# Performance work log

Hardware: AMD Instinct MI355X
Metric: run time of the kernel (lower is better)

Reference implementation:

```python
import jax, jax.numpy as jnp
import numpy as np

B, S, H, NH, HD = 2, 2048, 1024, 16, 64
RD = 16            # rotary_dim = head_dim * 0.25
W = 16             # mini_context_length (sliding window)
SCALE = HD ** -0.5
ROPE_BASE = 10000.0


def setup_inputs() -> dict:
    key = jax.random.key(0)
    ks = jax.random.split(key, 10)
    p = lambda k, shape: (jax.random.normal(k, shape, dtype=jnp.float32) * 0.02)
    return {
        "hidden_states": jax.random.normal(ks[0], (B, S, H), dtype=jnp.float32),
        "Wqkv": p(ks[1], (3 * H, H)), "bqkv": p(ks[2], (3 * H,)),
        "Wqa": p(ks[3], (H, H)),      "bqa": p(ks[4], (H,)),
        "Wka": p(ks[5], (H, H)),      "bka": p(ks[6], (H,)),
        "Wd": p(ks[7], (H, H)),       "bd": p(ks[8], (H,)),
    }


def _rotate_half(x):
    x1, x2 = jnp.split(x, 2, axis=-1)
    return jnp.concatenate([-x2, x1], axis=-1)


def _apply_rope(q, k, seq_len):
    # GPT-NeoX style rotary on the first RD dims. q,k: [B,NH,S,RD]
    inv_freq = 1.0 / (ROPE_BASE ** (jnp.arange(0, RD, 2, dtype=jnp.float32) / RD))
    t = jnp.arange(seq_len, dtype=jnp.float32)
    freqs = jnp.outer(t, inv_freq)                     # [S, RD//2]
    emb = jnp.concatenate([freqs, freqs], axis=-1)     # [S, RD]
    cos = jnp.cos(emb)[None, None]                      # [1,1,S,RD]
    sin = jnp.sin(emb)[None, None]
    return q * cos + _rotate_half(q) * sin, k * cos + _rotate_half(k) * sin


def reference(hidden_states, Wqkv, bqkv, Wqa, bqa, Wka, bka, Wd, bd):
    b, s, _ = hidden_states.shape
    qkv = hidden_states @ Wqkv.T + bqkv                       # [B,S,3H]
    qkv = qkv.reshape(b, s, 3, NH, HD).transpose(2, 0, 3, 1, 4)
    q, k, v = qkv[0], qkv[1], qkv[2]                          # [B,NH,S,HD]

    q_rot, k_rot = _apply_rope(q[..., :RD], k[..., :RD], s)
    q = jnp.concatenate([q_rot, q[..., RD:]], axis=-1)
    k = jnp.concatenate([k_rot, k[..., RD:]], axis=-1)

    # ----- Stage 1: sliding-window local attention (vectorized) -----
    pos = jnp.arange(s)
    idx = pos[:, None] - (W - 1) + jnp.arange(W)[None, :]     # [S,W]
    valid = idx >= 0
    idxc = jnp.clip(idx, 0, s - 1)
    k_win = k[:, :, idxc, :]                                   # [B,NH,S,W,HD]
    v_win = v[:, :, idxc, :]
    scores = jnp.einsum('bhsd,bhswd->bhsw', q, k_win) * SCALE
    scores = jnp.where(valid[None, None], scores, -jnp.inf)
    probs = jax.nn.softmax(scores, axis=-1)
    A = jnp.einsum('bhsw,bhswd->bhsd', probs, v_win)           # [B,NH,S,HD]

    A_hidden = A.transpose(0, 2, 1, 3).reshape(b, s, H)        # [B,S,H]

    # ----- Stage 2: causal global attention over A -----
    qa = (A_hidden @ Wqa.T + bqa).reshape(b, s, NH, HD).transpose(0, 2, 1, 3)
    ka = (A_hidden @ Wka.T + bka).reshape(b, s, NH, HD).transpose(0, 2, 1, 3)
    g = jnp.einsum('bhqd,bhkd->bhqk', qa, ka) * SCALE          # [B,NH,S,S]
    causal = pos[:, None] >= pos[None, :]
    g = jnp.where(causal[None, None], g, -jnp.inf)
    pg = jax.nn.softmax(g, axis=-1)
    out = jnp.einsum('bhqk,bhkd->bhqd', pg, A)                 # [B,NH,S,HD]
    out = out.transpose(0, 2, 1, 3).reshape(b, s, H)
    return out @ Wd.T + bd
```

## Files before the change

kernel.cpp:

```cpp
#include <hip/hip_runtime.h>
#include <hip/hip_bf16.h>
#include <cstdint>
#include <cstddef>

typedef __bf16 bf16;
typedef __bf16 bf16x4 __attribute__((ext_vector_type(4)));
typedef __bf16 bf16x8 __attribute__((ext_vector_type(8)));
typedef float  f32x4  __attribute__((ext_vector_type(4)));

#define DEVINL __device__ __forceinline__

constexpr int   Bc  = 2, Sc = 2048, Hc = 1024, NHc = 16, HDc = 64;
constexpr int   Tc  = Bc * Sc;
constexpr float L2E = 1.44269504088896340736f;
constexpr float NEG_BIG = -1.0e30f;

typedef __attribute__((address_space(1))) void AS1void;
typedef __attribute__((address_space(3))) void AS3void;

DEVINL void load_lds16(const bf16* g, bf16* l) {
  __builtin_amdgcn_global_load_lds((AS1void*)g, (AS3void*)l, 16, 0, 0);
}


__global__ __launch_bounds__(256)
void convert_all(const float* __restrict__ hs, const float* __restrict__ Wqkv,
                 const float* __restrict__ Wqa, const float* __restrict__ Wka,
                 const float* __restrict__ Wd, const float* __restrict__ bqa,
                 const float* __restrict__ bka,
                 bf16* __restrict__ hsb, bf16* __restrict__ wqkvb,
                 bf16* __restrict__ wqakab, bf16* __restrict__ wdb,
                 float* __restrict__ bqaka) {
  const int blk = blockIdx.x;
  if (blk >= 5120) {
    const int i = threadIdx.x * 8;
    const float* src = (i < 1024) ? (bqa + i) : (bka + i - 1024);
    *(f32x4*)(bqaka + i)     = *(const f32x4*)src;
    *(f32x4*)(bqaka + i + 4) = *(const f32x4*)(src + 4);
    return;
  }
  const float* src; bf16* dst; int base;
  if      (blk < 2048) { src = hs;   dst = hsb;                    base = blk; }
  else if (blk < 3584) { src = Wqkv; dst = wqkvb;                  base = blk - 2048; }
  else if (blk < 4096) { src = Wqa;  dst = wqakab;                 base = blk - 3584; }
  else if (blk < 4608) { src = Wka;  dst = wqakab + 1024 * 1024;   base = blk - 4096; }
  else                 { src = Wd;   dst = wdb;                    base = blk - 4608; }
  const int i = (base * 256 + threadIdx.x) * 8;
  f32x4 a = *(const f32x4*)(src + i);
  f32x4 b = *(const f32x4*)(src + i + 4);
  bf16x8 v;
#pragma unroll
  for (int j = 0; j < 4; j++) { v[j] = (bf16)a[j]; v[4 + j] = (bf16)b[j]; }
  *(bf16x8*)(dst + i) = v;
}

template <typename CT>
__global__ __launch_bounds__(256, 3)
void gemm128(const bf16* __restrict__ A, const bf16* __restrict__ Bw,
             const float* __restrict__ bias, CT* __restrict__ C,
             int M, int N, int K) {
  __shared__ __attribute__((aligned(16))) bf16 As[128 * 64];
  __shared__ __attribute__((aligned(16))) bf16 Bs[128 * 64];

  const int tid = threadIdx.x, wv = tid >> 6, lane = tid & 63;
  const int m0 = blockIdx.y * 128, n0 = blockIdx.x * 128;
  const int col = lane & 15, quad = lane >> 4;
  const int wrow = (wv >> 1) * 64, wcol = (wv & 1) * 64;

  f32x4 acc[4][4];
#pragma unroll
  for (int i = 0; i < 4; i++)
#pragma unroll
    for (int j = 0; j < 4; j++) acc[i][j] = f32x4{0.f, 0.f, 0.f, 0.f};

  const int srow = tid >> 3;
  const int scol = (((tid & 7) ^ (srow & 7)) << 3);
  const bf16* Ag = A  + (size_t)(m0 + srow) * K + scol;
  const bf16* Bg = Bw + (size_t)(n0 + srow) * K + scol;
  const int cs = col & 7;

  for (int k0 = 0; k0 < K; k0 += 64) {
#pragma unroll
    for (int c = 0; c < 4; c++) {
      load_lds16(Ag + (size_t)(c * 32) * K + k0, As + c * 2048 + tid * 8);
      load_lds16(Bg + (size_t)(c * 32) * K + k0, Bs + c * 2048 + tid * 8);
    }
    __syncthreads();
#pragma unroll
    for (int kk = 0; kk < 64; kk += 32) {
      const int so = ((((kk >> 3) + quad) ^ cs) << 3);
      bf16x8 af[4], bfr[4];
#pragma unroll
      for (int i = 0; i < 4; i++)
        af[i] = *(const bf16x8*)(As + (wrow + i * 16 + col) * 64 + so);
#pragma unroll
      for (int j = 0; j < 4; j++)
        bfr[j] = *(const bf16x8*)(Bs + (wcol + j * 16 + col) * 64 + so);
#pragma unroll
      for (int i = 0; i < 4; i++)
#pragma unroll
        for (int j = 0; j < 4; j++)
          acc[i][j] = __builtin_amdgcn_mfma_f32_16x16x32_bf16(af[i], bfr[j], acc[i][j], 0, 0, 0);
    }
    __syncthreads();
  }

#pragma unroll
  for (int j = 0; j < 4; j++) {
    const int c = n0 + wcol + j * 16 + col;
    const float bv = bias[c];
#pragma unroll
    for (int i = 0; i < 4; i++)
#pragma unroll
      for (int r = 0; r < 4; r++) {
        const int rr = m0 + wrow + i * 16 + quad * 4 + r;
        C[(size_t)rr * N + c] = (CT)(acc[i][j][r] + bv);
      }
  }
}

template <typename CT>
__global__ __launch_bounds__(256, 4)
void gemm6464(const bf16* __restrict__ A, const bf16* __restrict__ Bw,
              const float* __restrict__ bias, CT* __restrict__ C,
              int M, int N, int K) {
  __shared__ __attribute__((aligned(16))) bf16 As[64 * 64];
  __shared__ __attribute__((aligned(16))) bf16 Bs[64 * 64];

  const int tid = threadIdx.x, wv = tid >> 6, lane = tid & 63;
  const int m0 = blockIdx.y * 64, n0 = blockIdx.x * 64;
  const int col = lane & 15, quad = lane >> 4;

  f32x4 acc[4];
#pragma unroll
  for (int j = 0; j < 4; j++) acc[j] = f32x4{0.f, 0.f, 0.f, 0.f};

  const int srow = tid >> 3;
  const int scol = (((tid & 7) ^ (srow & 7)) << 3);
  const bf16* Ag = A  + (size_t)(m0 + srow) * K + scol;
  const bf16* Bg = Bw + (size_t)(n0 + srow) * K + scol;
  const int cs = col & 7;

  for (int k0 = 0; k0 < K; k0 += 64) {
#pragma unroll
    for (int c = 0; c < 2; c++) {
      load_lds16(Ag + (size_t)(c * 32) * K + k0, As + c * 2048 + tid * 8);
      load_lds16(Bg + (size_t)(c * 32) * K + k0, Bs + c * 2048 + tid * 8);
    }
    __syncthreads();
#pragma unroll
    for (int kk = 0; kk < 64; kk += 32) {
      const int so = ((((kk >> 3) + quad) ^ cs) << 3);
      bf16x8 af = *(const bf16x8*)(As + (wv * 16 + col) * 64 + so);
#pragma unroll
      for (int j = 0; j < 4; j++) {
        bf16x8 bfr = *(const bf16x8*)(Bs + (j * 16 + col) * 64 + so);
        acc[j] = __builtin_amdgcn_mfma_f32_16x16x32_bf16(af, bfr, acc[j], 0, 0, 0);
      }
    }
    __syncthreads();
  }

#pragma unroll
  for (int j = 0; j < 4; j++) {
    const int c = n0 + j * 16 + col;
    const float bv = bias[c];
#pragma unroll
    for (int r = 0; r < 4; r++) {
      const int rr = m0 + wv * 16 + quad * 4 + r;
      C[(size_t)rr * N + c] = (CT)(acc[j][r] + bv);
    }
  }
}

__global__ __launch_bounds__(256)
void window_attn(const bf16* __restrict__ qkv, bf16* __restrict__ Ah,
                 bf16* __restrict__ VTg) {
  __shared__ __attribute__((aligned(16))) bf16 Kw[31 * 72];
  __shared__ __attribute__((aligned(16))) bf16 Vw[31 * 72];
  const int g  = blockIdx.x;
  const int st = g & 127;
  const int h  = (g >> 7) & 15;
  const int b  = g >> 11;
  const int s0 = st * 16;
  const int tid = threadIdx.x;

  if ((tid < 124) || (tid >= 128 && tid < 252)) {
    const bool isK = tid < 124;
    const int lt  = isK ? tid : tid - 128;
    const int r   = lt >> 2, off = (lt & 3) << 4;
    int sidx = s0 - 15 + r; if (sidx < 0) sidx = 0;
    const bf16* src = qkv + (size_t)(b * Sc + sidx) * 3072 + (isK ? 1024 : 2048) + h * 64 + off;
    bf16x8 v0 = *(const bf16x8*)src;
    bf16x8 v1 = *(const bf16x8*)(src + 8);
    if (isK && off == 0) {
#pragma unroll
      for (int j = 0; j < 8; j++) {
        const float invf = exp2f(-(float)j * 1.66096404744368128f);
        float sn, csn;
        sincosf((float)sidx * invf, &sn, &csn);
        const float x1 = (float)v0[j], x2 = (float)v1[j];
        v0[j] = (bf16)(x1 * csn - x2 * sn);
        v1[j] = (bf16)(x2 * csn + x1 * sn);
      }
    }
    bf16* dst = (isK ? Kw : Vw) + r * 72 + off;
    *(bf16x8*)dst       = v0;
    *(bf16x8*)(dst + 8) = v1;
  }
  __syncthreads();

  const int wv = tid >> 6, lane = tid & 63;
  const int subq = lane >> 4, lane16 = lane & 15;
  const int s = s0 + wv * 4 + subq;
  const int t = b * Sc + s;
  const int d0 = lane16 * 4;

  float qd[4];
  {
    bf16x4 qv = *(const bf16x4*)(qkv + (size_t)t * 3072 + h * 64 + d0);
#pragma unroll
    for (int j = 0; j < 4; j++) qd[j] = (float)qv[j];
  }
  float pd[4];
#pragma unroll
  for (int j = 0; j < 4; j++) pd[j] = __shfl_xor(qd[j], 2, 64);
  if (lane16 < 4) {
#pragma unroll
    for (int j = 0; j < 4; j++) {
      const int jabs = d0 + j;
      const float invf = exp2f(-(float)(jabs & 7) * 1.66096404744368128f);
      float sn, csn;
      sincosf((float)s * invf, &sn, &csn);
      qd[j] = (jabs < 8) ? (qd[j] * csn - pd[j] * sn) : (qd[j] * csn + pd[j] * sn);
    }
  }

  float sc[16];
#pragma unroll
  for (int w = 0; w < 16; w++) {
    const int idxp = s - 15 + w;
    const int row = idxp - s0 + 15;
    bf16x4 kv = *(const bf16x4*)(Kw + row * 72 + d0);
    float p = qd[0] * (float)kv[0] + qd[1] * (float)kv[1] +
              qd[2] * (float)kv[2] + qd[3] * (float)kv[3];
#pragma unroll
    for (int m = 1; m < 16; m <<= 1) p += __shfl_xor(p, m, 64);
    sc[w] = (idxp < 0) ? NEG_BIG : p * 0.125f;
  }
  float mx = sc[0];
#pragma unroll
  for (int w = 1; w < 16; w++) mx = fmaxf(mx, sc[w]);
  float sum = 0.f;
#pragma unroll
  for (int w = 0; w < 16; w++) { sc[w] = exp2f((sc[w] - mx) * L2E); sum += sc[w]; }
  const float inv = 1.0f / fmaxf(sum, 1e-30f);

  float acc[4] = {0.f, 0.f, 0.f, 0.f};
#pragma unroll
  for (int w = 0; w < 16; w++) {
    const int idxp = s - 15 + w;
    const int row = idxp - s0 + 15;
    bf16x4 vv = *(const bf16x4*)(Vw + row * 72 + d0);
#pragma unroll
    for (int j = 0; j < 4; j++) acc[j] += sc[w] * (float)vv[j];
  }
  bf16x4 ov;
#pragma unroll
  for (int j = 0; j < 4; j++) ov[j] = (bf16)(acc[j] * inv);
  *(bf16x4*)(Ah + (size_t)t * 1024 + h * 64 + d0) = ov;
  bf16* vt = VTg + (((size_t)(b * 16 + h)) * 64 + d0) * 2048 + s;
#pragma unroll
  for (int j = 0; j < 4; j++) vt[(size_t)j * 2048] = ov[j];
}

__global__ __launch_bounds__(256, 4)
void flash_attn(const bf16* __restrict__ Q, const bf16* __restrict__ Kt,
                const bf16* __restrict__ VTg, bf16* __restrict__ O) {
  constexpr int QS = 2048;
  constexpr float SHIFT = 16.0f;
  __shared__ __attribute__((aligned(16))) bf16 K_lds[128 * 64];
  __shared__ __attribute__((aligned(16))) bf16 VT_lds[64 * 128];

  const int tid = threadIdx.x, wv = tid >> 6, lane = tid & 63;
  const int bh = blockIdx.x;
  const int y  = blockIdx.y;
  const int gq = y & 7, kq = y >> 3;
  const int qt = (kq == 0) ? gq : (kq == 1) ? (15 - gq)
               : (kq == 2) ? (16 + gq) : (31 - gq);
  const int b = bh >> 4, h = bh & 15;
  const int col = lane & 15, quad = lane >> 4;
  const size_t bS = (size_t)b * Sc;
  const int hd = h * 64;

  const int krow = tid >> 3;
  const int kcol = (((tid & 7) ^ (krow & 7)) << 3);
  const int vrow = tid >> 4;
  const int vcol = (((tid & 15) ^ vrow) << 3);
  const int cs8 = col & 7;

  const int qbase = qt * 64 + wv * 16;
  const int nkt = (qt + 2) >> 1;

  const bf16* qptr = Q + (bS + qbase + col) * QS + hd + quad * 8;
  bf16x8 qf[2];
  qf[0] = *(const bf16x8*)qptr;
  qf[1] = *(const bf16x8*)(qptr + 32);
#pragma unroll
  for (int hh = 0; hh < 2; hh++)
#pragma unroll
    for (int j = 0; j < 8; j++) qf[hh][j] = (bf16)((float)qf[hh][j] * 0.125f);

  f32x4 oacc[4];
#pragma unroll
  for (int i = 0; i < 4; i++) oacc[i] = f32x4{0.f, 0.f, 0.f, 0.f};
  float lsum = 0.f;

  for (int kt0 = 0; kt0 < nkt; kt0++) {
    const int k0 = kt0 * 128;
#pragma unroll
    for (int c = 0; c < 4; c++) {
      load_lds16(Kt + (bS + k0 + c * 32 + krow) * QS + hd + kcol,
                 K_lds + c * 2048 + tid * 8);
      load_lds16(VTg + ((size_t)bh * 64 + c * 16 + vrow) * 2048 + k0 + vcol,
                 VT_lds + c * 2048 + tid * 8);
    }
    __syncthreads();

    f32x4 sacc[8];
#pragma unroll
    for (int sub = 0; sub < 8; sub++) {
      f32x4 a = f32x4{0.f, 0.f, 0.f, 0.f};
#pragma unroll
      for (int hh = 0; hh < 2; hh++) {
        const int so = (((hh * 4 + quad) ^ cs8) << 3);
        bf16x8 kf = *(const bf16x8*)(K_lds + (sub * 16 + col) * 64 + so);
        a = __builtin_amdgcn_mfma_f32_16x16x32_bf16(kf, qf[hh], a, 0, 0, 0);
      }
      sacc[sub] = a;
    }
    if (kt0 == nkt - 1) {
      const int qq = qbase + col;
#pragma unroll
      for (int sub = 0; sub < 8; sub++)
#pragma unroll
        for (int r = 0; r < 4; r++) {
          const int key = k0 + sub * 16 + quad * 4 + r;
          if (key > qq) sacc[sub][r] = NEG_BIG;
        }
    }
#pragma unroll
    for (int sub = 0; sub < 8; sub++)
#pragma unroll
      for (int r = 0; r < 4; r++) {
        sacc[sub][r] = exp2f(sacc[sub][r] * L2E - SHIFT);
        lsum += sacc[sub][r];
      }

#pragma unroll
    for (int t = 0; t < 4; t++) {
      uint32_t a0, a1, b0, b1;
      asm("v_cvt_pk_bf16_f32 %0, %1, %2"
          : "=v"(a0) : "v"(sacc[2 * t][0]), "v"(sacc[2 * t][1]));
      asm("v_cvt_pk_bf16_f32 %0, %1, %2"
          : "=v"(a1) : "v"(sacc[2 * t][2]), "v"(sacc[2 * t][3]));
      asm("v_cvt_pk_bf16_f32 %0, %1, %2"
          : "=v"(b0) : "v"(sacc[2 * t + 1][0]), "v"(sacc[2 * t + 1][1]));
      asm("v_cvt_pk_bf16_f32 %0, %1, %2"
          : "=v"(b1) : "v"(sacc[2 * t + 1][2]), "v"(sacc[2 * t + 1][3]));
      asm("v_permlane32_swap_b32 %0, %1" : "+v"(a0), "+v"(b0));
      asm("v_permlane16_swap_b32 %0, %1" : "+v"(a0), "+v"(b0));
      asm("v_permlane32_swap_b32 %0, %1" : "+v"(a1), "+v"(b1));
      asm("v_permlane16_swap_b32 %0, %1" : "+v"(a1), "+v"(b1));
      union { uint32_t u[4]; bf16x8 v; } pk;
      pk.u[0] = a0; pk.u[1] = a1; pk.u[2] = b0; pk.u[3] = b1;
      const int vso = (((4 * t + quad) ^ col) << 3);
#pragma unroll
      for (int nb = 0; nb < 4; nb++) {
        bf16x8 vf = *(const bf16x8*)(VT_lds + (nb * 16 + col) * 128 + vso);
        oacc[nb] = __builtin_amdgcn_mfma_f32_16x16x32_bf16(pk.v, vf, oacc[nb], 0, 0, 0);
      }
    }
    __syncthreads();
  }

  float tot = lsum;
  tot += __shfl_xor(tot, 16, 64);
  tot += __shfl_xor(tot, 32, 64);
  float lrow[4];
#pragma unroll
  for (int r = 0; r < 4; r++)
    lrow[r] = 1.0f / fmaxf(__shfl(tot, quad * 4 + r, 16), 1e-37f);

#pragma unroll
  for (int nb = 0; nb < 4; nb++)
#pragma unroll
    for (int r = 0; r < 4; r++) {
      const int qq = qbase + quad * 4 + r;
      O[(bS + qq) * 1024 + hd + nb * 16 + col] = (bf16)(oacc[nb][r] * lrow[r]);
    }
}

extern "C" void kernel_launch(void* const* d_in, const int* in_sizes, int n_in,
                              void* d_out, int out_size, void* d_ws, size_t ws_size,
                              hipStream_t stream) {
  (void)in_sizes; (void)n_in; (void)out_size; (void)ws_size;
  const float* hs   = (const float*)d_in[0];
  const float* Wqkv = (const float*)d_in[1];
  const float* bqkv = (const float*)d_in[2];
  const float* Wqa  = (const float*)d_in[3];
  const float* bqa  = (const float*)d_in[4];
  const float* Wka  = (const float*)d_in[5];
  const float* bka  = (const float*)d_in[6];
  const float* Wd   = (const float*)d_in[7];
  const float* bd   = (const float*)d_in[8];
  float* out = (float*)d_out;

  const size_t TH = (size_t)Tc * Hc;
  bf16* dob   = (bf16*)d_out;
  bf16* hsb   = dob;
  bf16* wqkvb = dob + TH;
  bf16* Ah    = dob;
  bf16* VTg   = dob + TH;
  bf16* ws     = (bf16*)d_ws;
  bf16* qkv    = ws;
  bf16* qaka   = ws;
  bf16* oh     = ws + 2 * TH;
  bf16* wqakab = ws + 3 * TH;
  bf16* wdb    = wqakab + 2 * 1024 * 1024;
  float* bqaka = (float*)(wdb + 1024 * 1024);

  convert_all<<<dim3(5121), 256, 0, stream>>>(hs, Wqkv, Wqa, Wka, Wd, bqa, bka,
                                              hsb, wqkvb, wqakab, wdb, bqaka);

  gemm128<bf16><<<dim3(24, 32), 256, 0, stream>>>(hsb, wqkvb, bqkv, qkv, Tc, 3 * Hc, Hc);
  window_attn<<<dim3(Tc * NHc / 16), 256, 0, stream>>>(qkv, Ah, VTg);
  gemm128<bf16><<<dim3(16, 32), 256, 0, stream>>>(Ah, wqakab, bqaka, qaka, Tc, 2 * Hc, Hc);
  flash_attn<<<dim3(Bc * NHc, 32), 256, 0, stream>>>(qaka, qaka + Hc, VTg, oh);
  gemm6464<float><<<dim3(16, 64), 256, 0, stream>>>(oh, wdb, bd, out, Tc, Hc, Hc);
}
```

Before: 225.0 us.

## Pair complementary query tiles per block and double-buffer K/V tiles in LDS

Each flash-attention block now processes two query tiles, y and 31-y, so every block runs a constant 17 key-tile iterations. This balances the causal triangle across blocks and halves the grid. The K and V^T LDS buffers are doubled so the next tile's async global-to-LDS load is issued before computing on the current one, overlapping memory with MFMA work. In exchange, per-block LDS doubles and launch bounds drop to 2 blocks per CU, which lowers occupancy, and the grid shrinks to 512 blocks.

```diff
diff --git a/kernel.cpp b/kernel.cpp
--- a/kernel.cpp
+++ b/kernel.cpp
@@ -274,20 +274,19 @@
   for (int j = 0; j < 4; j++) vt[(size_t)j * 2048] = ov[j];
 }
 
-__global__ __launch_bounds__(256, 4)
+__global__ __launch_bounds__(256, 2)
 void flash_attn(const bf16* __restrict__ Q, const bf16* __restrict__ Kt,
                 const bf16* __restrict__ VTg, bf16* __restrict__ O) {
   constexpr int QS = 2048;
   constexpr float SHIFT = 16.0f;
-  __shared__ __attribute__((aligned(16))) bf16 K_lds[128 * 64];
-  __shared__ __attribute__((aligned(16))) bf16 VT_lds[64 * 128];
+  __shared__ __attribute__((aligned(16))) bf16 K_lds[2][128 * 64];
+  __shared__ __attribute__((aligned(16))) bf16 VT_lds[2][64 * 128];
 
   const int tid = threadIdx.x, wv = tid >> 6, lane = tid & 63;
   const int bh = blockIdx.x;
   const int y  = blockIdx.y;
-  const int gq = y & 7, kq = y >> 3;
-  const int qt = (kq == 0) ? gq : (kq == 1) ? (15 - gq)
-               : (kq == 2) ? (16 + gq) : (31 - gq);
+  const int qtA = y, qtB = 31 - y;
+  const int nA = (qtA + 2) >> 1;
   const int b = bh >> 4, h = bh & 15;
   const int col = lane & 15, quad = lane >> 4;
   const size_t bS = (size_t)b * Sc;
@@ -299,47 +298,78 @@
   const int vcol = (((tid & 15) ^ vrow) << 3);
   const int cs8 = col & 7;
 
-  const int qbase = qt * 64 + wv * 16;
-  const int nkt = (qt + 2) >> 1;
-
-  const bf16* qptr = Q + (bS + qbase + col) * QS + hd + quad * 8;
-  bf16x8 qf[2];
-  qf[0] = *(const bf16x8*)qptr;
-  qf[1] = *(const bf16x8*)(qptr + 32);
-#pragma unroll
-  for (int hh = 0; hh < 2; hh++)
-#pragma unroll
-    for (int j = 0; j < 8; j++) qf[hh][j] = (bf16)((float)qf[hh][j] * 0.125f);
+  bf16x8 qA0, qA1, qB0, qB1;
+  {
+    const bf16* qpA = Q + (bS + qtA * 64 + wv * 16 + col) * QS + hd + quad * 8;
+    const bf16* qpB = Q + (bS + qtB * 64 + wv * 16 + col) * QS + hd + quad * 8;
+    qA0 = *(const bf16x8*)qpA;
+    qA1 = *(const bf16x8*)(qpA + 32);
+    qB0 = *(const bf16x8*)qpB;
+    qB1 = *(const bf16x8*)(qpB + 32);
+#pragma unroll
+    for (int j = 0; j < 8; j++) {
+      qA0[j] = (bf16)((float)qA0[j] * 0.125f);
+      qA1[j] = (bf16)((float)qA1[j] * 0.125f);
+      qB0[j] = (bf16)((float)qB0[j] * 0.125f);
+      qB1[j] = (bf16)((float)qB1[j] * 0.125f);
+    }
+  }
+
+  auto stage = [&](int bufi, int k0) {
+#pragma unroll
+    for (int c = 0; c < 4; c++) {
+      load_lds16(Kt + (bS + k0 + c * 32 + krow) * QS + hd + kcol,
+                 K_lds[bufi] + c * 2048 + tid * 8);
+      load_lds16(VTg + ((size_t)bh * 64 + c * 16 + vrow) * 2048 + k0 + vcol,
+                 VT_lds[bufi] + c * 2048 + tid * 8);
+    }
+  };
 
   f32x4 oacc[4];
 #pragma unroll
   for (int i = 0; i < 4; i++) oacc[i] = f32x4{0.f, 0.f, 0.f, 0.f};
   float lsum = 0.f;
 
-  for (int kt0 = 0; kt0 < nkt; kt0++) {
-    const int k0 = kt0 * 128;
-#pragma unroll
-    for (int c = 0; c < 4; c++) {
-      load_lds16(Kt + (bS + k0 + c * 32 + krow) * QS + hd + kcol,
-                 K_lds + c * 2048 + tid * 8);
-      load_lds16(VTg + ((size_t)bh * 64 + c * 16 + vrow) * 2048 + k0 + vcol,
-                 VT_lds + c * 2048 + tid * 8);
-    }
-    __syncthreads();
+  stage(0, 0);
+  __syncthreads();
+  int cur = 0;
+
+  for (int it = 0; it < 17; it++) {
+    const int seg  = (it >= nA);
+    const int kt   = seg ? (it - nA) : it;
+    const int nkt  = seg ? (17 - nA) : nA;
+    const int qt   = seg ? qtB : qtA;
+    const int k0   = kt * 128;
+    const int qbase = qt * 64 + wv * 16;
+
+    if (it + 1 < 17) {
+      const int kt2 = (it + 1 >= nA) ? (it + 1 - nA) : (it + 1);
+      stage(cur ^ 1, kt2 * 128);
+    }
+
+    bf16x8 q0, q1;
+    if (seg == 0) { q0 = qA0; q1 = qA1; } else { q0 = qB0; q1 = qB1; }
+
+    const bf16* Kl = K_lds[cur];
+    const bf16* Vl = VT_lds[cur];
 
     f32x4 sacc[8];
 #pragma unroll
     for (int sub = 0; sub < 8; sub++) {
       f32x4 a = f32x4{0.f, 0.f, 0.f, 0.f};
-#pragma unroll
-      for (int hh = 0; hh < 2; hh++) {
-        const int so = (((hh * 4 + quad) ^ cs8) << 3);
-        bf16x8 kf = *(const bf16x8*)(K_lds + (sub * 16 + col) * 64 + so);
-        a = __builtin_amdgcn_mfma_f32_16x16x32_bf16(kf, qf[hh], a, 0, 0, 0);
+      {
+        const int so = ((quad ^ cs8) << 3);
+        bf16x8 kf = *(const bf16x8*)(Kl + (sub * 16 + col) * 64 + so);
+        a = __builtin_amdgcn_mfma_f32_16x16x32_bf16(kf, q0, a, 0, 0, 0);
+      }
+      {
+        const int so = (((4 + quad) ^ cs8) << 3);
+        bf16x8 kf = *(const bf16x8*)(Kl + (sub * 16 + col) * 64 + so);
+        a = __builtin_amdgcn_mfma_f32_16x16x32_bf16(kf, q1, a, 0, 0, 0);
       }
       sacc[sub] = a;
     }
-    if (kt0 == nkt - 1) {
+    if (kt == nkt - 1) {
       const int qq = qbase + col;
 #pragma unroll
       for (int sub = 0; sub < 8; sub++)
@@ -377,28 +407,34 @@
       const int vso = (((4 * t + quad) ^ col) << 3);
 #pragma unroll
       for (int nb = 0; nb < 4; nb++) {
-        bf16x8 vf = *(const bf16x8*)(VT_lds + (nb * 16 + col) * 128 + vso);
+        bf16x8 vf = *(const bf16x8*)(Vl + (nb * 16 + col) * 128 + vso);
         oacc[nb] = __builtin_amdgcn_mfma_f32_16x16x32_bf16(pk.v, vf, oacc[nb], 0, 0, 0);
       }
     }
+
+    if (kt == nkt - 1) {
+      float tot = lsum;
+      tot += __shfl_xor(tot, 16, 64);
+      tot += __shfl_xor(tot, 32, 64);
+      float lrow[4];
+#pragma unroll
+      for (int r = 0; r < 4; r++)
+        lrow[r] = 1.0f / fmaxf(__shfl(tot, quad * 4 + r, 16), 1e-37f);
+#pragma unroll
+      for (int nb = 0; nb < 4; nb++)
+#pragma unroll
+        for (int r = 0; r < 4; r++) {
+          const int qq = qbase + quad * 4 + r;
+          O[(bS + qq) * 1024 + hd + nb * 16 + col] = (bf16)(oacc[nb][r] * lrow[r]);
+        }
+#pragma unroll
+      for (int i = 0; i < 4; i++) oacc[i] = f32x4{0.f, 0.f, 0.f, 0.f};
+      lsum = 0.f;
+    }
+
     __syncthreads();
-  }
-
-  float tot = lsum;
-  tot += __shfl_xor(tot, 16, 64);
-  tot += __shfl_xor(tot, 32, 64);
-  float lrow[4];
-#pragma unroll
-  for (int r = 0; r < 4; r++)
-    lrow[r] = 1.0f / fmaxf(__shfl(tot, quad * 4 + r, 16), 1e-37f);
-
-#pragma unroll
-  for (int nb = 0; nb < 4; nb++)
-#pragma unroll
-    for (int r = 0; r < 4; r++) {
-      const int qq = qbase + quad * 4 + r;
-      O[(bS + qq) * 1024 + hd + nb * 16 + col] = (bf16)(oacc[nb][r] * lrow[r]);
-    }
+    cur ^= 1;
+  }
 }
 
 extern "C" void kernel_launch(void* const* d_in, const int* in_sizes, int n_in,
@@ -436,6 +472,6 @@
   gemm128<bf16><<<dim3(24, 32), 256, 0, stream>>>(hsb, wqkvb, bqkv, qkv, Tc, 3 * Hc, Hc);
   window_attn<<<dim3(Tc * NHc / 16), 256, 0, stream>>>(qkv, Ah, VTg);
   gemm128<bf16><<<dim3(16, 32), 256, 0, stream>>>(Ah, wqakab, bqaka, qaka, Tc, 2 * Hc, Hc);
-  flash_attn<<<dim3(Bc * NHc, 32), 256, 0, stream>>>(qaka, qaka + Hc, VTg, oh);
+  flash_attn<<<dim3(Bc * NHc, 16), 256, 0, stream>>>(qaka, qaka + Hc, VTg, oh);
   gemm6464<float><<<dim3(16, 64), 256, 0, stream>>>(oh, wdb, bd, out, Tc, Hc, Hc);
 }
```

New measurement: 238.2 us. +5.8%, slower.
